# Performance work log

Measured on AMD Instinct MI355X. Metric: run time of the kernel, lower is better.

## Reference

```python
import jax, jax.numpy as jnp
import numpy as np

B, H, S, D = 4, 16, 2048, 64
NEG = -1e9  # matches torch masked_fill(-1000000000.0)

def setup_inputs() -> dict:
    key = jax.random.key(0)
    kq, kk, kv, km = jax.random.split(key, 4)
    q = jax.random.normal(kq, (B, H, S, D), dtype=jnp.float32)
    k = jax.random.normal(kk, (B, H, S, D), dtype=jnp.float32)
    v = jax.random.normal(kv, (B, H, S, D), dtype=jnp.float32)
    key_padding_mask = jax.random.bernoulli(km, 0.1, (B, S))
    return {"q": q, "k": k, "v": v, "key_padding_mask": key_padding_mask}

def reference(q, k, v, key_padding_mask):
    d_k = q.shape[-1]
    scale = 1.0 / jnp.sqrt(jnp.asarray(d_k, dtype=q.dtype))
    # [B,H,S,S]
    scores = jnp.einsum('bhqd,bhkd->bhqk', q, k) * scale
    scores = jnp.where(key_padding_mask[:, None, None, :], NEG, scores)
    attn = jax.nn.softmax(scores, axis=-1)  # dropout p=0.0 -> identity
    return jnp.einsum('bhqk,bhkd->bhqd', attn, v)
```

## Files before the change

### kernel.cpp

```cpp
#include <hip/hip_runtime.h>
#include <hip/hip_bf16.h>

#define SQ 2048
#define DD 64
#define NBH 64
#define KVB 64
#define NT (SQ / KVB)
#define REC 16384
#define VOFF 8192
#define SCL 0.18033688011112042f

typedef __attribute__((ext_vector_type(8))) short bf16x8;
typedef __attribute__((ext_vector_type(4))) float f32x4;
typedef __attribute__((ext_vector_type(16))) float f32x16;

__device__ __forceinline__ short f2bf(float f) {
  union { float f; unsigned u; } un; un.f = f;
  unsigned r = un.u + 0x7fffu + ((un.u >> 16) & 1u);
  return (short)(r >> 16);
}

__device__ __forceinline__ unsigned cvtpk(float lo, float hi) {
  unsigned d;
  asm("v_cvt_pk_bf16_f32 %0, %1, %2" : "=v"(d) : "v"(lo), "v"(hi));
  return d;
}

__device__ __forceinline__ void gld_lds16(const void* g, void* l) {
  __builtin_amdgcn_global_load_lds(
      (const __attribute__((address_space(1))) unsigned int*)g,
      (__attribute__((address_space(3))) unsigned int*)l, 16, 0, 0);
}

__device__ __forceinline__ f32x16 z16() {
  f32x16 z;
  #pragma unroll
  for (int i = 0; i < 16; ++i) z[i] = 0.f;
  return z;
}


__global__ __launch_bounds__(256)
void prepack(const float* __restrict__ Kg, const float* __restrict__ Vg,
             const int* __restrict__ maskg, char* __restrict__ img)
{
  __shared__ float vst[64][68];
  const int bh = blockIdx.y, t = blockIdx.x;
  const size_t base = ((size_t)bh * SQ + (size_t)t * KVB) * DD;
  const int r  = threadIdx.x >> 2;
  const int q4 = threadIdx.x & 3;
  const int c0 = q4 * 16;
  char* rec = img + ((size_t)bh * NT + t) * REC;
  const int* mrow = maskg + (size_t)(bh >> 4) * SQ + t * KVB;
  unsigned long long mb = __ballot(mrow[threadIdx.x & 63] != 0);

  {
    const float* g = Vg + base + (size_t)r * DD + c0;
    #pragma unroll
    for (int i = 0; i < 4; ++i)
      *(f32x4*)&vst[r][c0 + i * 4] = *(const f32x4*)&g[i * 4];
  }
  {
    const float* g = Kg + base + (size_t)r * DD + c0;
    float tv[16];
    #pragma unroll
    for (int i = 0; i < 4; ++i) *(f32x4*)&tv[i * 4] = *(const f32x4*)&g[i * 4];
    bf16x8 lo, hi8;
    #pragma unroll
    for (int j = 0; j < 8; ++j) { lo[j] = f2bf(tv[j]); hi8[j] = f2bf(tv[8 + j]); }
    char* p = rec + r * 128;
    *(bf16x8*)(p + (((2 * q4)     ^ (r & 7)) << 4)) = lo;
    *(bf16x8*)(p + (((2 * q4 + 1) ^ (r & 7)) << 4)) = hi8;
  }
  __syncthreads();
  {
    const int d = r;
    bf16x8 lo, hi8;
    #pragma unroll
    for (int j = 0; j < 8; ++j) {
      int k0 = 8 * q4 + (j & 3) + 32 * ((j >> 2) & 1);
      int k1 = k0 + 4;
      lo[j]  = ((mb >> k0) & 1ull) ? (short)0 : f2bf(vst[k0][d]);
      hi8[j] = ((mb >> k1) & 1ull) ? (short)0 : f2bf(vst[k1][d]);
    }
    char* p = rec + VOFF + d * 128;
    *(bf16x8*)(p + (((2 * q4)     ^ (d & 7)) << 4)) = lo;
    *(bf16x8*)(p + (((2 * q4 + 1) ^ (d & 7)) << 4)) = hi8;
  }
}

__global__ __launch_bounds__(256)
void attn32(const char* __restrict__ img, const float* __restrict__ Qg,
            const int* __restrict__ maskg, float* __restrict__ Og)
{
  __shared__ char buf[2][REC];
  __shared__ __align__(16) short mones[NT][KVB];

  const int tid  = threadIdx.x;
  const int wv   = tid >> 6;
  const int lane = tid & 63;
  const int l31  = lane & 31;
  const int hi   = lane >> 5;

  const int bid = blockIdx.x;
  const int swz = (bid & 7) * 128 + (bid >> 3);
  const int qb = swz & 15;
  const int bh = swz >> 4;
  const int q0 = qb * 128 + wv * 32;
  const size_t base = (size_t)bh * SQ * DD;
  const char* rec0 = img + (size_t)bh * NT * REC;

  {
    const int* mrow = maskg + (size_t)(bh >> 4) * SQ;
    #pragma unroll
    for (int i = 0; i < 8; ++i) {
      int idx = tid + i * 256;
      int t = idx >> 6, p = idx & 63;
      int kv = 8 * (p >> 4) + 4 * ((p >> 3) & 1) + (p & 3) + 32 * ((p >> 2) & 1);
      mones[t][p] = mrow[t * KVB + kv] ? (short)0 : (short)0x3F80;
    }
  }

  int slotoff[4];
  #pragma unroll
  for (int kk = 0; kk < 4; ++kk)
    slotoff[kk] = (((2 * kk + hi) ^ (l31 & 7)) << 4);
  const int rbase = l31 * 128;

  bf16x8 qf[4];
  {
    const float* qrow = Qg + base + (size_t)(q0 + l31) * DD + hi * 8;
    #pragma unroll
    for (int kk = 0; kk < 4; ++kk) {
      float tv[8];
      *(f32x4*)&tv[0] = *(const f32x4*)&qrow[kk * 16];
      *(f32x4*)&tv[4] = *(const f32x4*)&qrow[kk * 16 + 4];
      #pragma unroll
      for (int j = 0; j < 8; ++j) qf[kk][j] = f2bf(tv[j] * SCL);
    }
  }

  #pragma unroll
  for (int i = 0; i < 4; ++i)
    gld_lds16(rec0 + i * 4096 + tid * 16, buf[0] + i * 4096 + tid * 16);

  f32x16 accO0 = z16(), accO1 = z16(), acc2 = z16();

  int cur = 0;
  for (int t = 0; t < NT; ++t) {
    asm volatile("s_waitcnt vmcnt(0)" ::: "memory");
    __syncthreads();

    if (t + 1 < NT) {
      const char* rec = rec0 + (size_t)(t + 1) * REC;
      char* dst = buf[cur ^ 1];
      #pragma unroll
      for (int i = 0; i < 4; ++i)
        gld_lds16(rec + i * 4096 + tid * 16, dst + i * 4096 + tid * 16);
    }

    const char* bk = buf[cur];
    f32x16 sA = z16(), sB = z16();
    __builtin_amdgcn_s_setprio(1);
    #pragma unroll
    for (int kk = 0; kk < 4; ++kk) {
      bf16x8 k0 = *(const bf16x8*)(bk + rbase + slotoff[kk]);
      bf16x8 k1 = *(const bf16x8*)(bk + 4096 + rbase + slotoff[kk]);
      sA = __builtin_amdgcn_mfma_f32_32x32x16_bf16(k0, qf[kk], sA, 0, 0, 0);
      sB = __builtin_amdgcn_mfma_f32_32x32x16_bf16(k1, qf[kk], sB, 0, 0, 0);
    }
    __builtin_amdgcn_s_setprio(0);

    #pragma unroll
    for (int r = 0; r < 16; ++r) {
      sA[r] = exp2f(sA[r]);
      sB[r] = exp2f(sB[r]);
    }

    const short* mrowt = &mones[t][0];
    __builtin_amdgcn_s_setprio(1);
    #pragma unroll
    for (int kk = 0; kk < 4; ++kk) {
      union { unsigned u[4]; bf16x8 v; } pf;
      pf.u[0] = cvtpk(sA[4 * kk + 0], sA[4 * kk + 1]);
      pf.u[1] = cvtpk(sA[4 * kk + 2], sA[4 * kk + 3]);
      pf.u[2] = cvtpk(sB[4 * kk + 0], sB[4 * kk + 1]);
      pf.u[3] = cvtpk(sB[4 * kk + 2], sB[4 * kk + 3]);
      bf16x8 vf0 = *(const bf16x8*)(bk + VOFF + rbase + slotoff[kk]);
      bf16x8 vf1 = *(const bf16x8*)(bk + VOFF + 4096 + rbase + slotoff[kk]);
      bf16x8 of  = *(const bf16x8*)(mrowt + (2 * kk + hi) * 8);
      accO0 = __builtin_amdgcn_mfma_f32_32x32x16_bf16(pf.v, vf0, accO0, 0, 0, 0);
      accO1 = __builtin_amdgcn_mfma_f32_32x32x16_bf16(pf.v, vf1, accO1, 0, 0, 0);
      acc2  = __builtin_amdgcn_mfma_f32_32x32x16_bf16(pf.v, of,  acc2,  0, 0, 0);
    }
    __builtin_amdgcn_s_setprio(0);
    cur ^= 1;
  }

  #pragma unroll
  for (int reg = 0; reg < 16; ++reg) {
    int ql = (reg & 3) + 8 * (reg >> 2) + 4 * hi;
    float iq = 1.0f / acc2[reg];
    float* orow = Og + base + (size_t)(q0 + ql) * DD;
    orow[l31]      = accO0[reg] * iq;
    orow[32 + l31] = accO1[reg] * iq;
  }
}

__global__ __launch_bounds__(256)
void attn_fallback(const float* __restrict__ Qg, const float* __restrict__ Kg,
                   const float* __restrict__ Vg, const int* __restrict__ maskg,
                   float* __restrict__ Og)
{
  __shared__ short ktf[KVB][72];
  __shared__ short vtf[DD][72];
  __shared__ short ptf[4][16][72];
  __shared__ float bias_s[KVB];

  const int tid = threadIdx.x, wv = tid >> 6, lane = tid & 63;
  const int l15 = lane & 15, lg = lane >> 4;
  const int bh = blockIdx.y, bb = bh >> 4, q0 = blockIdx.x * 64;
  const size_t base = (size_t)bh * SQ * DD;
  const f32x4 zero4 = {0.f, 0.f, 0.f, 0.f};

  bf16x8 qf[2];
  {
    const float* qrow = Qg + base + (size_t)(q0 + wv * 16 + l15) * DD + lg * 8;
    #pragma unroll
    for (int kf = 0; kf < 2; ++kf) {
      float tv[8];
      *(f32x4*)&tv[0] = *(const f32x4*)&qrow[kf * 32];
      *(f32x4*)&tv[4] = *(const f32x4*)&qrow[kf * 32 + 4];
      #pragma unroll
      for (int j = 0; j < 8; ++j) qf[kf][j] = f2bf(tv[j]);
    }
  }
  f32x4 oacc[4];
  #pragma unroll
  for (int d = 0; d < 4; ++d) oacc[d] = zero4;
  float mrun[4] = {-3e38f, -3e38f, -3e38f, -3e38f};
  float lrun[4] = {0.f, 0.f, 0.f, 0.f};

  for (int kv0 = 0; kv0 < SQ; kv0 += KVB) {
    __syncthreads();
    {
      int r = tid >> 2, c0 = (tid & 3) * 16;
      const float* g = Kg + base + (size_t)(kv0 + r) * DD + c0;
      float tv[16];
      #pragma unroll
      for (int i = 0; i < 4; ++i) *(f32x4*)&tv[i * 4] = *(const f32x4*)&g[i * 4];
      bf16x8 a, b2;
      #pragma unroll
      for (int j = 0; j < 8; ++j) { a[j] = f2bf(tv[j]); b2[j] = f2bf(tv[8 + j]); }
      *(bf16x8*)&ktf[r][c0] = a;
      *(bf16x8*)&ktf[r][c0 + 8] = b2;
    }
    {
      int r = tid & 63, c0 = (tid >> 6) * 16;
      const float* g = Vg + base + (size_t)(kv0 + r) * DD + c0;
      float tv[16];
      #pragma unroll
      for (int i = 0; i < 4; ++i) *(f32x4*)&tv[i * 4] = *(const f32x4*)&g[i * 4];
      #pragma unroll
      for (int j = 0; j < 16; ++j) vtf[c0 + j][r] = f2bf(tv[j]);
    }
    if (tid < KVB) bias_s[tid] = maskg[(size_t)bb * SQ + kv0 + tid] ? -1e9f : 0.f;
    __syncthreads();

    f32x4 acc[4];
    #pragma unroll
    for (int n = 0; n < 4; ++n) acc[n] = zero4;
    #pragma unroll
    for (int n = 0; n < 4; ++n) {
      bf16x8 k0 = *(const bf16x8*)&ktf[n * 16 + l15][lg * 8];
      bf16x8 k1 = *(const bf16x8*)&ktf[n * 16 + l15][32 + lg * 8];
      acc[n] = __builtin_amdgcn_mfma_f32_16x16x32_bf16(qf[0], k0, acc[n], 0, 0, 0);
      acc[n] = __builtin_amdgcn_mfma_f32_16x16x32_bf16(qf[1], k1, acc[n], 0, 0, 0);
    }
    float brow[4];
    #pragma unroll
    for (int n = 0; n < 4; ++n) brow[n] = bias_s[n * 16 + l15];
    #pragma unroll
    for (int reg = 0; reg < 4; ++reg) {
      float s0 = acc[0][reg] * 0.125f + brow[0];
      float s1 = acc[1][reg] * 0.125f + brow[1];
      float s2 = acc[2][reg] * 0.125f + brow[2];
      float s3 = acc[3][reg] * 0.125f + brow[3];
      float tm = fmaxf(fmaxf(s0, s1), fmaxf(s2, s3));
      #pragma unroll
      for (int off = 1; off < 16; off <<= 1) tm = fmaxf(tm, __shfl_xor(tm, off, 64));
      float mnew = fmaxf(mrun[reg], tm);
      float scale = __expf(mrun[reg] - mnew);
      float p0 = __expf(s0 - mnew), p1 = __expf(s1 - mnew);
      float p2 = __expf(s2 - mnew), p3 = __expf(s3 - mnew);
      float rs = (p0 + p1) + (p2 + p3);
      #pragma unroll
      for (int off = 1; off < 16; off <<= 1) rs += __shfl_xor(rs, off, 64);
      lrun[reg] = lrun[reg] * scale + rs;
      mrun[reg] = mnew;
      #pragma unroll
      for (int d = 0; d < 4; ++d) oacc[d][reg] *= scale;
      int prow = lg * 4 + reg;
      ptf[wv][prow][     l15] = f2bf(p0);
      ptf[wv][prow][16 + l15] = f2bf(p1);
      ptf[wv][prow][32 + l15] = f2bf(p2);
      ptf[wv][prow][48 + l15] = f2bf(p3);
    }
    bf16x8 pf0 = *(const bf16x8*)&ptf[wv][l15][lg * 8];
    bf16x8 pf1 = *(const bf16x8*)&ptf[wv][l15][32 + lg * 8];
    #pragma unroll
    for (int d = 0; d < 4; ++d) {
      bf16x8 v0 = *(const bf16x8*)&vtf[d * 16 + l15][lg * 8];
      bf16x8 v1 = *(const bf16x8*)&vtf[d * 16 + l15][32 + lg * 8];
      oacc[d] = __builtin_amdgcn_mfma_f32_16x16x32_bf16(pf0, v0, oacc[d], 0, 0, 0);
      oacc[d] = __builtin_amdgcn_mfma_f32_16x16x32_bf16(pf1, v1, oacc[d], 0, 0, 0);
    }
  }
  #pragma unroll
  for (int reg = 0; reg < 4; ++reg) {
    float inv = 1.0f / lrun[reg];
    int row = q0 + wv * 16 + lg * 4 + reg;
    float* orow = Og + base + (size_t)row * DD;
    #pragma unroll
    for (int d = 0; d < 4; ++d) orow[d * 16 + l15] = oacc[d][reg] * inv;
  }
}

extern "C" void kernel_launch(void* const* d_in, const int* in_sizes, int n_in,
                              void* d_out, int out_size, void* d_ws, size_t ws_size,
                              hipStream_t stream) {
  const float* q    = (const float*)d_in[0];
  const float* k    = (const float*)d_in[1];
  const float* v    = (const float*)d_in[2];
  const int*   mask = (const int*)d_in[3];
  float* out = (float*)d_out;

  const size_t need = (size_t)NBH * NT * REC;
  if (ws_size >= need) {
    char* img = (char*)d_ws;
    dim3 pgrid(NT, NBH);
    prepack<<<pgrid, 256, 0, stream>>>(k, v, mask, img);
    attn32<<<dim3(1024), 256, 0, stream>>>(img, q, mask, out);
  } else {
    dim3 grid(SQ / 64, NBH);
    attn_fallback<<<grid, 256, 0, stream>>>(q, k, v, mask, out);
  }
}
```

Before: 140.0 us.

## Process two 32-row query tiles per wave to reuse each staged K/V tile

Each wave now handles 64 query rows (two 32-row sub-tiles) instead of 32, so every block covers 256 queries and the grid halves to 512 blocks. Each K/V tile loaded into LDS is reused for twice as many queries, which halves global/LDS staging traffic and barrier count per query. The cost is doubled accumulator and Q-fragment registers, which may lower occupancy. On 256 CUs the 512 blocks also give fewer waves in flight to hide latency.

Result: slower. 192.7 us (+37.7%).

```diff
diff --git a/kernel.cpp b/kernel.cpp
--- a/kernel.cpp
+++ b/kernel.cpp
@@ -103,10 +103,10 @@
   const int hi   = lane >> 5;
 
   const int bid = blockIdx.x;
-  const int swz = (bid & 7) * 128 + (bid >> 3);
-  const int qb = swz & 15;
-  const int bh = swz >> 4;
-  const int q0 = qb * 128 + wv * 32;
+  const int swz = (bid & 7) * 64 + (bid >> 3);
+  const int qb = swz & 7;
+  const int bh = swz >> 3;
+  const int q0 = qb * 256 + wv * 64;
   const size_t base = (size_t)bh * SQ * DD;
   const char* rec0 = img + (size_t)bh * NT * REC;
 
@@ -127,16 +127,17 @@
     slotoff[kk] = (((2 * kk + hi) ^ (l31 & 7)) << 4);
   const int rbase = l31 * 128;
 
-  bf16x8 qf[4];
-  {
-    const float* qrow = Qg + base + (size_t)(q0 + l31) * DD + hi * 8;
+  bf16x8 qf[2][4];
+  #pragma unroll
+  for (int s = 0; s < 2; ++s) {
+    const float* qrow = Qg + base + (size_t)(q0 + s * 32 + l31) * DD + hi * 8;
     #pragma unroll
     for (int kk = 0; kk < 4; ++kk) {
       float tv[8];
       *(f32x4*)&tv[0] = *(const f32x4*)&qrow[kk * 16];
       *(f32x4*)&tv[4] = *(const f32x4*)&qrow[kk * 16 + 4];
       #pragma unroll
-      for (int j = 0; j < 8; ++j) qf[kk][j] = f2bf(tv[j] * SCL);
+      for (int j = 0; j < 8; ++j) qf[s][kk][j] = f2bf(tv[j] * SCL);
     }
   }
 
@@ -144,7 +145,8 @@
   for (int i = 0; i < 4; ++i)
     gld_lds16(rec0 + i * 4096 + tid * 16, buf[0] + i * 4096 + tid * 16);
 
-  f32x16 accO0 = z16(), accO1 = z16(), acc2 = z16();
+  f32x16 accO00 = z16(), accO01 = z16(), acc20 = z16();
+  f32x16 accO10 = z16(), accO11 = z16(), acc21 = z16();
 
   int cur = 0;
   for (int t = 0; t < NT; ++t) {
@@ -160,50 +162,68 @@
     }
 
     const char* bk = buf[cur];
-    f32x16 sA = z16(), sB = z16();
-    __builtin_amdgcn_s_setprio(1);
-    #pragma unroll
-    for (int kk = 0; kk < 4; ++kk) {
-      bf16x8 k0 = *(const bf16x8*)(bk + rbase + slotoff[kk]);
-      bf16x8 k1 = *(const bf16x8*)(bk + 4096 + rbase + slotoff[kk]);
-      sA = __builtin_amdgcn_mfma_f32_32x32x16_bf16(k0, qf[kk], sA, 0, 0, 0);
-      sB = __builtin_amdgcn_mfma_f32_32x32x16_bf16(k1, qf[kk], sB, 0, 0, 0);
-    }
-    __builtin_amdgcn_s_setprio(0);
-
-    #pragma unroll
-    for (int r = 0; r < 16; ++r) {
-      sA[r] = exp2f(sA[r]);
-      sB[r] = exp2f(sB[r]);
-    }
-
     const short* mrowt = &mones[t][0];
-    __builtin_amdgcn_s_setprio(1);
-    #pragma unroll
-    for (int kk = 0; kk < 4; ++kk) {
-      union { unsigned u[4]; bf16x8 v; } pf;
-      pf.u[0] = cvtpk(sA[4 * kk + 0], sA[4 * kk + 1]);
-      pf.u[1] = cvtpk(sA[4 * kk + 2], sA[4 * kk + 3]);
-      pf.u[2] = cvtpk(sB[4 * kk + 0], sB[4 * kk + 1]);
-      pf.u[3] = cvtpk(sB[4 * kk + 2], sB[4 * kk + 3]);
-      bf16x8 vf0 = *(const bf16x8*)(bk + VOFF + rbase + slotoff[kk]);
-      bf16x8 vf1 = *(const bf16x8*)(bk + VOFF + 4096 + rbase + slotoff[kk]);
-      bf16x8 of  = *(const bf16x8*)(mrowt + (2 * kk + hi) * 8);
-      accO0 = __builtin_amdgcn_mfma_f32_32x32x16_bf16(pf.v, vf0, accO0, 0, 0, 0);
-      accO1 = __builtin_amdgcn_mfma_f32_32x32x16_bf16(pf.v, vf1, accO1, 0, 0, 0);
-      acc2  = __builtin_amdgcn_mfma_f32_32x32x16_bf16(pf.v, of,  acc2,  0, 0, 0);
-    }
-    __builtin_amdgcn_s_setprio(0);
+
+    #pragma unroll
+    for (int s = 0; s < 2; ++s) {
+      f32x16 sA = z16(), sB = z16();
+      __builtin_amdgcn_s_setprio(1);
+      #pragma unroll
+      for (int kk = 0; kk < 4; ++kk) {
+        bf16x8 k0 = *(const bf16x8*)(bk + rbase + slotoff[kk]);
+        bf16x8 k1 = *(const bf16x8*)(bk + 4096 + rbase + slotoff[kk]);
+        sA = __builtin_amdgcn_mfma_f32_32x32x16_bf16(k0, qf[s][kk], sA, 0, 0, 0);
+        sB = __builtin_amdgcn_mfma_f32_32x32x16_bf16(k1, qf[s][kk], sB, 0, 0, 0);
+      }
+      __builtin_amdgcn_s_setprio(0);
+
+      #pragma unroll
+      for (int r = 0; r < 16; ++r) {
+        sA[r] = exp2f(sA[r]);
+        sB[r] = exp2f(sB[r]);
+      }
+
+      __builtin_amdgcn_s_setprio(1);
+      #pragma unroll
+      for (int kk = 0; kk < 4; ++kk) {
+        union { unsigned u[4]; bf16x8 v; } pf;
+        pf.u[0] = cvtpk(sA[4 * kk + 0], sA[4 * kk + 1]);
+        pf.u[1] = cvtpk(sA[4 * kk + 2], sA[4 * kk + 3]);
+        pf.u[2] = cvtpk(sB[4 * kk + 0], sB[4 * kk + 1]);
+        pf.u[3] = cvtpk(sB[4 * kk + 2], sB[4 * kk + 3]);
+        bf16x8 vf0 = *(const bf16x8*)(bk + VOFF + rbase + slotoff[kk]);
+        bf16x8 vf1 = *(const bf16x8*)(bk + VOFF + 4096 + rbase + slotoff[kk]);
+        bf16x8 of  = *(const bf16x8*)(mrowt + (2 * kk + hi) * 8);
+        if (s == 0) {
+          accO00 = __builtin_amdgcn_mfma_f32_32x32x16_bf16(pf.v, vf0, accO00, 0, 0, 0);
+          accO01 = __builtin_amdgcn_mfma_f32_32x32x16_bf16(pf.v, vf1, accO01, 0, 0, 0);
+          acc20  = __builtin_amdgcn_mfma_f32_32x32x16_bf16(pf.v, of,  acc20,  0, 0, 0);
+        } else {
+          accO10 = __builtin_amdgcn_mfma_f32_32x32x16_bf16(pf.v, vf0, accO10, 0, 0, 0);
+          accO11 = __builtin_amdgcn_mfma_f32_32x32x16_bf16(pf.v, vf1, accO11, 0, 0, 0);
+          acc21  = __builtin_amdgcn_mfma_f32_32x32x16_bf16(pf.v, of,  acc21,  0, 0, 0);
+        }
+      }
+      __builtin_amdgcn_s_setprio(0);
+    }
     cur ^= 1;
   }
 
   #pragma unroll
   for (int reg = 0; reg < 16; ++reg) {
     int ql = (reg & 3) + 8 * (reg >> 2) + 4 * hi;
-    float iq = 1.0f / acc2[reg];
-    float* orow = Og + base + (size_t)(q0 + ql) * DD;
-    orow[l31]      = accO0[reg] * iq;
-    orow[32 + l31] = accO1[reg] * iq;
+    {
+      float iq = 1.0f / acc20[reg];
+      float* orow = Og + base + (size_t)(q0 + ql) * DD;
+      orow[l31]      = accO00[reg] * iq;
+      orow[32 + l31] = accO01[reg] * iq;
+    }
+    {
+      float iq = 1.0f / acc21[reg];
+      float* orow = Og + base + (size_t)(q0 + 32 + ql) * DD;
+      orow[l31]      = accO10[reg] * iq;
+      orow[32 + l31] = accO11[reg] * iq;
+    }
   }
 }
 
@@ -340,7 +360,7 @@
     char* img = (char*)d_ws;
     dim3 pgrid(NT, NBH);
     prepack<<<pgrid, 256, 0, stream>>>(k, v, mask, img);
-    attn32<<<dim3(1024), 256, 0, stream>>>(img, q, mask, out);
+    attn32<<<dim3(512), 256, 0, stream>>>(img, q, mask, out);
   } else {
     dim3 grid(SQ / 64, NBH);
     attn_fallback<<<grid, 256, 0, stream>>>(q, k, v, mask, out);
```
